# Optimization experiments

Hardware: AMD Instinct MI355X
Metric: run time of the kernel (lower is better)

Reference implementation:

```python
import jax, jax.numpy as jnp
import numpy as np
from jax import lax

B, NCH, T = 256, 32, 2000
NTF, NSF, NSUB, TK = 4, 40, 20, 25
NCLS = 4
NTAN = NSUB * (NSUB + 1) // 2
REIG_EPS = 1e-4


def setup_inputs() -> dict:
    key = jax.random.key(0)
    ks = jax.random.split(key, 8)
    x = jax.random.normal(ks[0], (B, NCH, T), dtype=jnp.float32)
    conv1_w = jax.random.normal(ks[1], (NTF, 1, 1, TK), dtype=jnp.float32) * 0.2
    conv1_b = jnp.zeros((NTF,), dtype=jnp.float32)
    conv2_w = jax.random.normal(ks[2], (NSF, NTF, NCH, 1), dtype=jnp.float32) * 0.1
    conv2_b = jnp.zeros((NSF,), dtype=jnp.float32)
    # BiMap weight: semi-orthogonal (n_subspace x n_spatial_filters) via QR
    A = jax.random.normal(ks[3], (NSF, NSUB), dtype=jnp.float32)
    Q, _ = jnp.linalg.qr(A)
    W_bimap = Q.T  # (NSUB, NSF), rows orthonormal
    clf_w = jax.random.normal(ks[4], (NCLS, NTAN), dtype=jnp.float32) * 0.05
    clf_b = jnp.zeros((NCLS,), dtype=jnp.float32)
    return {"x": x, "conv1_w": conv1_w, "conv1_b": conv1_b,
            "conv2_w": conv2_w, "conv2_b": conv2_b,
            "W_bimap": W_bimap, "clf_w": clf_w, "clf_b": clf_b}


def _forward(x, conv1_w, conv1_b, conv2_w, conv2_b, W_bimap, clf_w, clf_b):
    dn = ('NCHW', 'OIHW', 'NCHW')
    h = x[:, None, :, :]  # (B,1,NCH,T)
    # temporal conv, 'same' with reflect padding along time
    pl = (TK - 1) // 2
    pr = TK - 1 - pl
    hp = jnp.pad(h, ((0, 0), (0, 0), (0, 0), (pl, pr)), mode='reflect')
    h1 = lax.conv_general_dilated(hp, conv1_w, (1, 1), 'VALID', dimension_numbers=dn)
    h1 = h1 + conv1_b[None, :, None, None]  # (B,NTF,NCH,T)
    # spatial conv collapses channel axis
    h2 = lax.conv_general_dilated(h1, conv2_w, (1, 1), 'VALID', dimension_numbers=dn)
    h2 = h2 + conv2_b[None, :, None, None]  # (B,NSF,1,T)
    h2 = h2.reshape(B, NSF, T)
    # covariance pooling over time (unbiased)
    hm = h2 - h2.mean(axis=-1, keepdims=True)
    C = jnp.einsum('bft,bgt->bfg', hm, hm) / (T - 1)  # (B,NSF,NSF)
    # BiMap: S = W C W^T  -> (B,NSUB,NSUB)
    S = jnp.einsum('if,bfg,jg->bij', W_bimap, C, W_bimap)
    # ReEig: clamp eigenvalues at threshold
    w, U = jnp.linalg.eigh(S)
    w = jnp.maximum(w, REIG_EPS)
    S = jnp.einsum('bik,bk,bjk->bij', U, w, U)
    # LogEig: matrix log, take scaled upper triangle, flatten
    w2, U2 = jnp.linalg.eigh(S)
    L = jnp.einsum('bik,bk,bjk->bij', U2, jnp.log(w2), U2)
    iu, ju = jnp.triu_indices(NSUB)
    scale = jnp.where(iu == ju, 1.0, jnp.sqrt(2.0)).astype(L.dtype)
    z = L[:, iu, ju] * scale[None, :]  # (B, NTAN)
    return z @ clf_w.T + clf_b


def reference(x, conv1_w, conv1_b, conv2_w, conv2_b, W_bimap, clf_w, clf_b):
    return _forward(x, conv1_w, conv1_b, conv2_w, conv2_b, W_bimap, clf_w, clf_b)
```

## Files before the change

### kernel.cpp

```cpp
#include <hip/hip_runtime.h>
#include <math.h>

#define B_    256
#define NCH   32
#define T_    2000
#define NTF   4
#define NSF   40
#define NSUB  20
#define TK    25
#define NCLS  4
#define NTAN  210
#define NPAIR 820
#define ACC_STRIDE 860
#define TILE_T 250
#define NTILE  8
#define PL     12

#define ACC_FLOATS (B_*ACC_STRIDE)
#define W2T_OFF ACC_FLOATS
#define W1T_OFF (ACC_FLOATS + NSF*NTF*NCH)

#define XS_TSTR 36
#define H2_STR  252
#define LDS_DW  10080

typedef float v2f __attribute__((ext_vector_type(2)));

__device__ __forceinline__ v2f fma2(v2f a, v2f b, v2f c) {
#if __has_builtin(__builtin_elementwise_fma)
    return __builtin_elementwise_fma(a, b, c);
#else
    v2f r; r.x = fmaf(a.x, b.x, c.x); r.y = fmaf(a.y, b.y, c.y); return r;
#endif
}

__device__ __forceinline__ int pack_ut(int f, int g) {
    return f*NSF - (f*(f-1))/2 + (g - f);
}

__global__ void prep_kernel(const float* __restrict__ conv1_w,
                            const float* __restrict__ conv2_w,
                            float* __restrict__ ws) {
    int tid = threadIdx.x;
    float* w2t = ws + W2T_OFF;
    float* w1t = ws + W1T_OFF;
    for (int i = tid; i < NSF*NTF*NCH; i += 256) {
        int f  = i & 3;
        int sc = i >> 2;
        int c  = sc & 31;
        int s  = sc >> 5;
        w2t[i] = conv2_w[(s*NTF + f)*NCH + c];
    }
    for (int i = tid; i < NTF*TK; i += 256) {
        int f = i & 3;
        int k = i >> 2;
        w1t[i] = conv1_w[f*TK + k];
    }
}

__global__ __launch_bounds__(256, 2)
void conv_gram_kernel(const float* __restrict__ x,
                      const float* __restrict__ conv1_b,
                      const float* __restrict__ conv2_b,
                      const float* __restrict__ wts,
                      float* __restrict__ acc)
{
    __shared__ float lds[LDS_DW];

    const int tid  = threadIdx.x;
    const int bid  = blockIdx.x;
    const int b    = bid >> 3;
    const int tile = bid & 7;
    const int t0   = tile * TILE_T;

    const float* xb = x + (size_t)b*NCH*T_;
    for (int li = tid; li < NCH*280; li += 256) {
        int c = li / 280;
        int i = li - c*280;
        int tg = t0 + i - PL;
        tg = (tg < 0) ? -tg : tg;
        tg = (tg >= T_) ? (2*T_ - 2 - tg) : tg;
        lds[i*XS_TSTR + c] = xb[c*T_ + tg];
    }
    __syncthreads();

    const float4* w1t = (const float4*)(wts + W1T_OFF);
    const float4* w2t = (const float4*)(wts + W2T_OFF);

    v2f h1[64];
    {
        float b0 = conv1_b[0], b1 = conv1_b[1], b2 = conv1_b[2], b3 = conv1_b[3];
        #pragma unroll
        for (int c = 0; c < NCH; ++c) {
            v2f lo; lo.x = b0; lo.y = b1;
            v2f hi; hi.x = b2; hi.y = b3;
            h1[2*c]   = lo;
            h1[2*c+1] = hi;
        }
    }
    #pragma clang loop unroll(disable)
    for (int k = 0; k < TK; ++k) {
        float4 wq = w1t[k];
        v2f w01; w01.x = wq.x; w01.y = wq.y;
        v2f w23; w23.x = wq.z; w23.y = wq.w;
        const float4* xr = (const float4*)&lds[(tid + k)*XS_TSTR];
        float4 xv4[8];
        #pragma unroll
        for (int j = 0; j < 8; ++j) xv4[j] = xr[j];
        const float* xv = (const float*)xv4;
        #pragma unroll
        for (int c = 0; c < NCH; ++c) {
            v2f xc; xc.x = xv[c]; xc.y = xv[c];
            h1[2*c]   = fma2(xc, w01, h1[2*c]);
            h1[2*c+1] = fma2(xc, w23, h1[2*c+1]);
        }
    }
    __syncthreads();

    #pragma clang loop unroll_count(2)
    for (int s = 0; s < NSF; ++s) {
        v2f a01; a01.x = conv2_b[s]; a01.y = 0.f;
        v2f a23; a23.x = 0.f;        a23.y = 0.f;
        #pragma unroll
        for (int c = 0; c < NCH; ++c) {
            float4 wq = w2t[s*NCH + c];
            v2f w01; w01.x = wq.x; w01.y = wq.y;
            v2f w23; w23.x = wq.z; w23.y = wq.w;
            a01 = fma2(w01, h1[2*c],   a01);
            a23 = fma2(w23, h1[2*c+1], a23);
        }
        float v = (a01.x + a01.y) + (a23.x + a23.y);
        if (tid < H2_STR) lds[s*H2_STR + tid] = (tid < TILE_T) ? v : 0.f;
    }
    __syncthreads();

    float* accb = acc + b*ACC_STRIDE;

    if (tid < 55) {
        int bf = 0, rem = tid;
        while (rem >= 10 - bf) { rem -= 10 - bf; bf++; }
        int bg = bf + rem;

        const float4* rA[4];
        const float4* rB[4];
        #pragma unroll
        for (int a = 0; a < 4; ++a) {
            rA[a] = (const float4*)&lds[(4*bf + a)*H2_STR];
            rB[a] = (const float4*)&lds[(4*bg + a)*H2_STR];
        }
        v2f accL[16], accH[16];
        #pragma unroll
        for (int i = 0; i < 16; ++i) { accL[i] = (v2f)0.f; accH[i] = (v2f)0.f; }

        #pragma unroll 7
        for (int q = 0; q < H2_STR/4; ++q) {
            float4 av[4], bv[4];
            #pragma unroll
            for (int a = 0; a < 4; ++a) av[a] = rA[a][q];
            #pragma unroll
            for (int a = 0; a < 4; ++a) bv[a] = rB[a][q];
            #pragma unroll
            for (int a = 0; a < 4; ++a) {
                v2f aL; aL.x = av[a].x; aL.y = av[a].y;
                v2f aH; aH.x = av[a].z; aH.y = av[a].w;
                #pragma unroll
                for (int g = 0; g < 4; ++g) {
                    v2f bL; bL.x = bv[g].x; bL.y = bv[g].y;
                    v2f bH; bH.x = bv[g].z; bH.y = bv[g].w;
                    accL[a*4+g] = fma2(aL, bL, accL[a*4+g]);
                    accH[a*4+g] = fma2(aH, bH, accH[a*4+g]);
                }
            }
        }
        #pragma unroll
        for (int a = 0; a < 4; ++a) {
            #pragma unroll
            for (int g = 0; g < 4; ++g) {
                int f  = 4*bf + a;
                int gg = 4*bg + g;
                if (f <= gg) {
                    v2f sL = accL[a*4+g], sH = accH[a*4+g];
                    float s = (sL.x + sL.y) + (sH.x + sH.y);
                    atomicAdd(&accb[pack_ut(f, gg)], s);
                }
            }
        }
    }

    if (tid >= 64 && tid < 64 + NSF) {
        int row = tid - 64;
        const float4* rr = (const float4*)&lds[row*H2_STR];
        float csum = 0.f;
        #pragma unroll 7
        for (int q = 0; q < H2_STR/4; ++q) {
            float4 v = rr[q];
            csum += (v.x + v.y) + (v.z + v.w);
        }
        atomicAdd(&accb[NPAIR + row], csum);
    }
}

__device__ __forceinline__ void pq_sched(int r, int k, int& p, int& q) {
    if (k == 0) { p = 19; q = r; }
    else {
        int a = r + k;      if (a >= 19) a -= 19;
        int d = r - k + 19; if (d >= 19) d -= 19;
        p = a; q = d;
    }
}

__global__ __launch_bounds__(128)
void finalize_kernel(const float* __restrict__ acc,
                     const float* __restrict__ W_bimap,
                     const float* __restrict__ clf_w,
                     const float* __restrict__ clf_b,
                     float* __restrict__ out)
{
    __shared__ float C[NSF*NSF];
    __shared__ float Wb[NSUB*NSF];
    __shared__ float M[NSUB*NSF];
    __shared__ float A[NSUB*21];
    __shared__ float V[NSUB*21];
    __shared__ float cs_c[10], cs_s[10];
    __shared__ float lam[NSUB];
    __shared__ float z[NTAN];

    const int tid = threadIdx.x;
    const int b   = blockIdx.x;
    const float* accb = acc + b*ACC_STRIDE;

    for (int i = tid; i < NSF*NSF; i += 128) {
        int f = i / NSF, g = i % NSF;
        int lo = f < g ? f : g;
        int hi = f < g ? g : f;
        double G  = (double)accb[pack_ut(lo, hi)];
        double sf = (double)accb[NPAIR + f];
        double sg = (double)accb[NPAIR + g];
        C[i] = (float)((G - sf*sg/(double)T_) / (double)(T_ - 1));
    }
    for (int i = tid; i < NSUB*NSF; i += 128) Wb[i] = W_bimap[i];
    __syncthreads();

    for (int i = tid; i < NSUB*NSF; i += 128) {
        int r = i / NSF, g = i % NSF;
        float s = 0.f;
        #pragma unroll 8
        for (int f = 0; f < NSF; ++f) s = fmaf(Wb[r*NSF+f], C[f*NSF+g], s);
        M[i] = s;
    }
    __syncthreads();

    for (int i = tid; i < NSUB*NSUB; i += 128) {
        int r = i / NSUB, j = i % NSUB;
        float s = 0.f;
        #pragma unroll 8
        for (int g = 0; g < NSF; ++g) s = fmaf(M[r*NSF+g], Wb[j*NSF+g], s);
        A[r*21+j] = s;
        V[r*21+j] = (r == j) ? 1.f : 0.f;
    }
    __syncthreads();

    const int kk = tid / 10;
    const int ll = tid - 10*(tid/10);

    for (int sweep = 0; sweep < 7; ++sweep) {
        for (int r = 0; r < 19; ++r) {
            if (tid < 10) {
                int p, q; pq_sched(r, tid, p, q);
                float app = A[p*21+p], aqq = A[q*21+q], apq = A[p*21+q];
                float c = 1.f, s = 0.f;
                if (fabsf(apq) > 1e-30f) {
                    float tau = (aqq - app) / (2.f*apq);
                    float t = 1.f / (fabsf(tau) + sqrtf(1.f + tau*tau));
                    if (tau < 0.f) t = -t;
                    c = 1.f / sqrtf(1.f + t*t);
                    s = t * c;
                }
                cs_c[tid] = c; cs_s[tid] = s;
            }
            __syncthreads();
            if (tid < 100) {
                int pk, qk, pl, ql;
                pq_sched(r, kk, pk, qk);
                pq_sched(r, ll, pl, ql);
                float ck = cs_c[kk], sk = cs_s[kk];
                float cl = cs_c[ll], sl = cs_s[ll];
                float a00 = A[pk*21+pl], a01 = A[pk*21+ql];
                float a10 = A[qk*21+pl], a11 = A[qk*21+ql];
                float t00 = ck*a00 - sk*a10, t01 = ck*a01 - sk*a11;
                float t10 = sk*a00 + ck*a10, t11 = sk*a01 + ck*a11;
                A[pk*21+pl] = cl*t00 - sl*t01;
                A[pk*21+ql] = sl*t00 + cl*t01;
                A[qk*21+pl] = cl*t10 - sl*t11;
                A[qk*21+ql] = sl*t10 + cl*t11;
                float v00 = V[pk*21+pl], v01 = V[pk*21+ql];
                float v10 = V[qk*21+pl], v11 = V[qk*21+ql];
                V[pk*21+pl] = cl*v00 - sl*v01;
                V[pk*21+ql] = sl*v00 + cl*v01;
                V[qk*21+pl] = cl*v10 - sl*v11;
                V[qk*21+ql] = sl*v10 + cl*v11;
            }
            __syncthreads();
        }
    }

    if (tid < NSUB) {
        float w = A[tid*21+tid];
        lam[tid] = logf(fmaxf(w, 1e-4f));
    }
    __syncthreads();

    for (int p = tid; p < NTAN; p += 128) {
        int i = 0, rem = p;
        while (rem >= NSUB - i) { rem -= NSUB - i; i++; }
        int j = i + rem;
        float s = 0.f;
        #pragma unroll 5
        for (int k = 0; k < NSUB; ++k) s = fmaf(V[i*21+k]*lam[k], V[j*21+k], s);
        z[p] = (i == j) ? s : s * 1.41421356237309515f;
    }
    __syncthreads();

    if (tid < NCLS) {
        float s = clf_b[tid];
        for (int p = 0; p < NTAN; ++p) s = fmaf(clf_w[tid*NTAN+p], z[p], s);
        out[b*NCLS + tid] = s;
    }
}

extern "C" void kernel_launch(void* const* d_in, const int* in_sizes, int n_in,
                              void* d_out, int out_size, void* d_ws, size_t ws_size,
                              hipStream_t stream) {
    const float* x       = (const float*)d_in[0];
    const float* conv1_w = (const float*)d_in[1];
    const float* conv1_b = (const float*)d_in[2];
    const float* conv2_w = (const float*)d_in[3];
    const float* conv2_b = (const float*)d_in[4];
    const float* W_bimap = (const float*)d_in[5];
    const float* clf_w   = (const float*)d_in[6];
    const float* clf_b   = (const float*)d_in[7];
    float* out = (float*)d_out;
    float* ws  = (float*)d_ws;

    hipMemsetAsync(ws, 0, (size_t)ACC_FLOATS*sizeof(float), stream);

    prep_kernel<<<1, 256, 0, stream>>>(conv1_w, conv2_w, ws);
    conv_gram_kernel<<<B_*NTILE, 256, 0, stream>>>(x, conv1_b, conv2_b, ws, ws);
    finalize_kernel<<<B_, 128, 0, stream>>>(ws, W_bimap, clf_w, clf_b, out);
}
```

Baseline: 329.4 us.

## Restructure conv into channel groups, split gram across 220 threads, single-wave Jacobi finalize

The conv stage now processes channels in groups of 8, folding each group's temporal conv straight into 40 running spatial-conv accumulators. This drops the 64-register h1 array, which should lower register pressure. The Gram stage now spreads the 55 tile pairs across four time chunks each (220 threads) instead of 55 threads, and the column sums likewise use 160 threads, at the cost of more atomics. The finalize kernel runs as a single 64-thread wave that computes rotation coefficients redundantly per thread with fast rcp/rsq intrinsics, which removes one barrier per Jacobi round. That last part may cost some precision.

Result: slower. 714.3 us (+116.8%).

```diff
diff --git a/kernel.cpp b/kernel.cpp
--- a/kernel.cpp
+++ b/kernel.cpp
@@ -21,8 +21,8 @@
 #define W1T_OFF (ACC_FLOATS + NSF*NTF*NCH)
 
 #define XS_TSTR 36
-#define H2_STR  252
-#define LDS_DW  10080
+#define H2_STR  260
+#define LDS_DW  10400
 
 typedef float v2f __attribute__((ext_vector_type(2)));
 
@@ -87,73 +87,90 @@
     const float4* w1t = (const float4*)(wts + W1T_OFF);
     const float4* w2t = (const float4*)(wts + W2T_OFF);
 
-    v2f h1[64];
-    {
-        float b0 = conv1_b[0], b1 = conv1_b[1], b2 = conv1_b[2], b3 = conv1_b[3];
+    float h2acc[NSF];
+    #pragma unroll
+    for (int s = 0; s < NSF; ++s) h2acc[s] = conv2_b[s];
+
+    const float b1_0 = conv1_b[0], b1_1 = conv1_b[1], b1_2 = conv1_b[2], b1_3 = conv1_b[3];
+
+    for (int g = 0; g < 4; ++g) {
+        v2f h1g[16];
         #pragma unroll
-        for (int c = 0; c < NCH; ++c) {
-            v2f lo; lo.x = b0; lo.y = b1;
-            v2f hi; hi.x = b2; hi.y = b3;
-            h1[2*c]   = lo;
-            h1[2*c+1] = hi;
-        }
-    }
-    #pragma clang loop unroll(disable)
-    for (int k = 0; k < TK; ++k) {
-        float4 wq = w1t[k];
-        v2f w01; w01.x = wq.x; w01.y = wq.y;
-        v2f w23; w23.x = wq.z; w23.y = wq.w;
-        const float4* xr = (const float4*)&lds[(tid + k)*XS_TSTR];
-        float4 xv4[8];
-        #pragma unroll
-        for (int j = 0; j < 8; ++j) xv4[j] = xr[j];
-        const float* xv = (const float*)xv4;
-        #pragma unroll
-        for (int c = 0; c < NCH; ++c) {
-            v2f xc; xc.x = xv[c]; xc.y = xv[c];
-            h1[2*c]   = fma2(xc, w01, h1[2*c]);
-            h1[2*c+1] = fma2(xc, w23, h1[2*c+1]);
-        }
-    }
-    __syncthreads();
-
-    #pragma clang loop unroll_count(2)
-    for (int s = 0; s < NSF; ++s) {
-        v2f a01; a01.x = conv2_b[s]; a01.y = 0.f;
-        v2f a23; a23.x = 0.f;        a23.y = 0.f;
-        #pragma unroll
-        for (int c = 0; c < NCH; ++c) {
-            float4 wq = w2t[s*NCH + c];
+        for (int c = 0; c < 8; ++c) {
+            v2f lo; lo.x = b1_0; lo.y = b1_1;
+            v2f hi; hi.x = b1_2; hi.y = b1_3;
+            h1g[2*c]   = lo;
+            h1g[2*c+1] = hi;
+        }
+        #pragma clang loop unroll(disable)
+        for (int k = 0; k < TK; ++k) {
+            float4 wq = w1t[k];
             v2f w01; w01.x = wq.x; w01.y = wq.y;
             v2f w23; w23.x = wq.z; w23.y = wq.w;
-            a01 = fma2(w01, h1[2*c],   a01);
-            a23 = fma2(w23, h1[2*c+1], a23);
-        }
-        float v = (a01.x + a01.y) + (a23.x + a23.y);
-        if (tid < H2_STR) lds[s*H2_STR + tid] = (tid < TILE_T) ? v : 0.f;
+            const float4* xp = (const float4*)&lds[(tid + k)*XS_TSTR + 8*g];
+            float4 xa = xp[0];
+            float4 xc = xp[1];
+            float xv0 = xa.x, xv1 = xa.y, xv2 = xa.z, xv3 = xa.w;
+            float xv4 = xc.x, xv5 = xc.y, xv6 = xc.z, xv7 = xc.w;
+            v2f t;
+            t.x = xv0; t.y = xv0; h1g[0]  = fma2(t, w01, h1g[0]);  h1g[1]  = fma2(t, w23, h1g[1]);
+            t.x = xv1; t.y = xv1; h1g[2]  = fma2(t, w01, h1g[2]);  h1g[3]  = fma2(t, w23, h1g[3]);
+            t.x = xv2; t.y = xv2; h1g[4]  = fma2(t, w01, h1g[4]);  h1g[5]  = fma2(t, w23, h1g[5]);
+            t.x = xv3; t.y = xv3; h1g[6]  = fma2(t, w01, h1g[6]);  h1g[7]  = fma2(t, w23, h1g[7]);
+            t.x = xv4; t.y = xv4; h1g[8]  = fma2(t, w01, h1g[8]);  h1g[9]  = fma2(t, w23, h1g[9]);
+            t.x = xv5; t.y = xv5; h1g[10] = fma2(t, w01, h1g[10]); h1g[11] = fma2(t, w23, h1g[11]);
+            t.x = xv6; t.y = xv6; h1g[12] = fma2(t, w01, h1g[12]); h1g[13] = fma2(t, w23, h1g[13]);
+            t.x = xv7; t.y = xv7; h1g[14] = fma2(t, w01, h1g[14]); h1g[15] = fma2(t, w23, h1g[15]);
+        }
+        #pragma unroll
+        for (int s = 0; s < NSF; ++s) {
+            v2f a2; a2.x = 0.f; a2.y = 0.f;
+            #pragma unroll
+            for (int c = 0; c < 8; ++c) {
+                float4 wq = w2t[s*NCH + 8*g + c];
+                v2f w01; w01.x = wq.x; w01.y = wq.y;
+                v2f w23; w23.x = wq.z; w23.y = wq.w;
+                a2 = fma2(w01, h1g[2*c],   a2);
+                a2 = fma2(w23, h1g[2*c+1], a2);
+            }
+            h2acc[s] += a2.x + a2.y;
+        }
+    }
+    __syncthreads();
+
+    #pragma unroll
+    for (int s = 0; s < NSF; ++s) {
+        float vw = (tid < TILE_T) ? h2acc[s] : 0.f;
+        lds[s*H2_STR + tid] = vw;
+    }
+    for (int i = tid; i < NSF*4; i += 256) {
+        int s = i >> 2, col = 256 + (i & 3);
+        lds[s*H2_STR + col] = 0.f;
     }
     __syncthreads();
 
     float* accb = acc + b*ACC_STRIDE;
 
-    if (tid < 55) {
-        int bf = 0, rem = tid;
+    if (tid < 220) {
+        int tilei = tid >> 2, chunk = tid & 3;
+        int bf = 0, rem = tilei;
         while (rem >= 10 - bf) { rem -= 10 - bf; bf++; }
         int bg = bf + rem;
+        int q0 = chunk * 16;
+        int qn = (chunk == 3) ? 17 : 16;
 
         const float4* rA[4];
         const float4* rB[4];
         #pragma unroll
         for (int a = 0; a < 4; ++a) {
-            rA[a] = (const float4*)&lds[(4*bf + a)*H2_STR];
-            rB[a] = (const float4*)&lds[(4*bg + a)*H2_STR];
+            rA[a] = (const float4*)&lds[(bf + 10*a)*H2_STR] + q0;
+            rB[a] = (const float4*)&lds[(bg + 10*a)*H2_STR] + q0;
         }
         v2f accL[16], accH[16];
         #pragma unroll
-        for (int i = 0; i < 16; ++i) { accL[i] = (v2f)0.f; accH[i] = (v2f)0.f; }
-
-        #pragma unroll 7
-        for (int q = 0; q < H2_STR/4; ++q) {
+        for (int i = 0; i < 16; ++i) { accL[i].x = 0.f; accL[i].y = 0.f; accH[i] = accL[i]; }
+
+        for (int q = 0; q < qn; ++q) {
             float4 av[4], bv[4];
             #pragma unroll
             for (int a = 0; a < 4; ++a) av[a] = rA[a][q];
@@ -164,39 +181,42 @@
                 v2f aL; aL.x = av[a].x; aL.y = av[a].y;
                 v2f aH; aH.x = av[a].z; aH.y = av[a].w;
                 #pragma unroll
-                for (int g = 0; g < 4; ++g) {
-                    v2f bL; bL.x = bv[g].x; bL.y = bv[g].y;
-                    v2f bH; bH.x = bv[g].z; bH.y = bv[g].w;
-                    accL[a*4+g] = fma2(aL, bL, accL[a*4+g]);
-                    accH[a*4+g] = fma2(aH, bH, accH[a*4+g]);
+                for (int gI = 0; gI < 4; ++gI) {
+                    v2f bL; bL.x = bv[gI].x; bL.y = bv[gI].y;
+                    v2f bH; bH.x = bv[gI].z; bH.y = bv[gI].w;
+                    accL[a*4+gI] = fma2(aL, bL, accL[a*4+gI]);
+                    accH[a*4+gI] = fma2(aH, bH, accH[a*4+gI]);
                 }
             }
         }
         #pragma unroll
         for (int a = 0; a < 4; ++a) {
             #pragma unroll
-            for (int g = 0; g < 4; ++g) {
-                int f  = 4*bf + a;
-                int gg = 4*bg + g;
-                if (f <= gg) {
-                    v2f sL = accL[a*4+g], sH = accH[a*4+g];
+            for (int gI = 0; gI < 4; ++gI) {
+                int f  = bf + 10*a;
+                int gg = bg + 10*gI;
+                if (bf != bg || a <= gI) {
+                    int lo = f < gg ? f : gg;
+                    int hi = f < gg ? gg : f;
+                    v2f sL = accL[a*4+gI], sH = accH[a*4+gI];
                     float s = (sL.x + sL.y) + (sH.x + sH.y);
-                    atomicAdd(&accb[pack_ut(f, gg)], s);
+                    atomicAdd(&accb[pack_ut(lo, hi)], s);
                 }
             }
         }
     }
 
-    if (tid >= 64 && tid < 64 + NSF) {
-        int row = tid - 64;
-        const float4* rr = (const float4*)&lds[row*H2_STR];
-        float csum = 0.f;
-        #pragma unroll 7
-        for (int q = 0; q < H2_STR/4; ++q) {
+    if (tid < 160) {
+        int row = tid >> 2, chunk = tid & 3;
+        int q0 = chunk * 16;
+        int qn = (chunk == 3) ? 17 : 16;
+        const float4* rr = (const float4*)&lds[row*H2_STR] + q0;
+        float cs = 0.f;
+        for (int q = 0; q < qn; ++q) {
             float4 v = rr[q];
-            csum += (v.x + v.y) + (v.z + v.w);
-        }
-        atomicAdd(&accb[NPAIR + row], csum);
+            cs += (v.x + v.y) + (v.z + v.w);
+        }
+        atomicAdd(&accb[NPAIR + row], cs);
     }
 }
 
@@ -209,7 +229,19 @@
     }
 }
 
-__global__ __launch_bounds__(128)
+__device__ __forceinline__ void rotcs(float app, float aqq, float apq,
+                                      float& c, float& s) {
+    if (fabsf(apq) > 1e-30f) {
+        float tau = (aqq - app) * __builtin_amdgcn_rcpf(2.f*apq);
+        float sq  = __builtin_amdgcn_sqrtf(fmaf(tau, tau, 1.f));
+        float t   = __builtin_amdgcn_rcpf(fabsf(tau) + sq);
+        t = (tau < 0.f) ? -t : t;
+        c = __builtin_amdgcn_rsqf(fmaf(t, t, 1.f));
+        s = t * c;
+    } else { c = 1.f; s = 0.f; }
+}
+
+__global__ __launch_bounds__(64)
 void finalize_kernel(const float* __restrict__ acc,
                      const float* __restrict__ W_bimap,
                      const float* __restrict__ clf_w,
@@ -221,7 +253,6 @@
     __shared__ float M[NSUB*NSF];
     __shared__ float A[NSUB*21];
     __shared__ float V[NSUB*21];
-    __shared__ float cs_c[10], cs_s[10];
     __shared__ float lam[NSUB];
     __shared__ float z[NTAN];
 
@@ -229,19 +260,19 @@
     const int b   = blockIdx.x;
     const float* accb = acc + b*ACC_STRIDE;
 
-    for (int i = tid; i < NSF*NSF; i += 128) {
+    for (int i = tid; i < NSF*NSF; i += 64) {
         int f = i / NSF, g = i % NSF;
         int lo = f < g ? f : g;
         int hi = f < g ? g : f;
         double G  = (double)accb[pack_ut(lo, hi)];
         double sf = (double)accb[NPAIR + f];
         double sg = (double)accb[NPAIR + g];
-        C[i] = (float)((G - sf*sg/(double)T_) / (double)(T_ - 1));
-    }
-    for (int i = tid; i < NSUB*NSF; i += 128) Wb[i] = W_bimap[i];
-    __syncthreads();
-
-    for (int i = tid; i < NSUB*NSF; i += 128) {
+        C[i] = (float)((G - sf*sg*(1.0/2000.0)) * (1.0/1999.0));
+    }
+    for (int i = tid; i < NSUB*NSF; i += 64) Wb[i] = W_bimap[i];
+    __syncthreads();
+
+    for (int i = tid; i < NSUB*NSF; i += 64) {
         int r = i / NSF, g = i % NSF;
         float s = 0.f;
         #pragma unroll 8
@@ -250,7 +281,7 @@
     }
     __syncthreads();
 
-    for (int i = tid; i < NSUB*NSUB; i += 128) {
+    for (int i = tid; i < NSUB*NSUB; i += 64) {
         int r = i / NSUB, j = i % NSUB;
         float s = 0.f;
         #pragma unroll 8
@@ -260,45 +291,67 @@
     }
     __syncthreads();
 
-    const int kk = tid / 10;
-    const int ll = tid - 10*(tid/10);
+    const int k0 = tid / 10, l0 = tid - 10*(tid/10);
+    const bool has1 = (tid < 36);
+    const int i1 = tid + 64;
+    const int k1 = i1 / 10, l1 = i1 - 10*(i1/10);
 
     for (int sweep = 0; sweep < 7; ++sweep) {
         for (int r = 0; r < 19; ++r) {
-            if (tid < 10) {
-                int p, q; pq_sched(r, tid, p, q);
-                float app = A[p*21+p], aqq = A[q*21+q], apq = A[p*21+q];
-                float c = 1.f, s = 0.f;
-                if (fabsf(apq) > 1e-30f) {
-                    float tau = (aqq - app) / (2.f*apq);
-                    float t = 1.f / (fabsf(tau) + sqrtf(1.f + tau*tau));
-                    if (tau < 0.f) t = -t;
-                    c = 1.f / sqrtf(1.f + t*t);
-                    s = t * c;
-                }
-                cs_c[tid] = c; cs_s[tid] = s;
-            }
-            __syncthreads();
-            if (tid < 100) {
-                int pk, qk, pl, ql;
-                pq_sched(r, kk, pk, qk);
-                pq_sched(r, ll, pl, ql);
-                float ck = cs_c[kk], sk = cs_s[kk];
-                float cl = cs_c[ll], sl = cs_s[ll];
-                float a00 = A[pk*21+pl], a01 = A[pk*21+ql];
-                float a10 = A[qk*21+pl], a11 = A[qk*21+ql];
-                float t00 = ck*a00 - sk*a10, t01 = ck*a01 - sk*a11;
-                float t10 = sk*a00 + ck*a10, t11 = sk*a01 + ck*a11;
-                A[pk*21+pl] = cl*t00 - sl*t01;
-                A[pk*21+ql] = sl*t00 + cl*t01;
-                A[qk*21+pl] = cl*t10 - sl*t11;
-                A[qk*21+ql] = sl*t10 + cl*t11;
-                float v00 = V[pk*21+pl], v01 = V[pk*21+ql];
-                float v10 = V[qk*21+pl], v11 = V[qk*21+ql];
-                V[pk*21+pl] = cl*v00 - sl*v01;
-                V[pk*21+ql] = sl*v00 + cl*v01;
-                V[qk*21+pl] = cl*v10 - sl*v11;
-                V[qk*21+ql] = sl*v10 + cl*v11;
+            int pk0, qk0, pl0, ql0, pk1, qk1, pl1, ql1;
+            pq_sched(r, k0, pk0, qk0);
+            pq_sched(r, l0, pl0, ql0);
+            pq_sched(r, k1, pk1, qk1);
+            pq_sched(r, l1, pl1, ql1);
+
+            float kpp0 = A[pk0*21+pk0], kqq0 = A[qk0*21+qk0], kpq0 = A[pk0*21+qk0];
+            float lpp0 = A[pl0*21+pl0], lqq0 = A[ql0*21+ql0], lpq0 = A[pl0*21+ql0];
+            float a00_0 = A[pk0*21+pl0], a01_0 = A[pk0*21+ql0];
+            float a10_0 = A[qk0*21+pl0], a11_0 = A[qk0*21+ql0];
+            float v00_0 = V[pk0*21+pl0], v01_0 = V[pk0*21+ql0];
+            float v10_0 = V[qk0*21+pl0], v11_0 = V[qk0*21+ql0];
+
+            float kpp1=0.f, kqq1=0.f, kpq1=0.f, lpp1=0.f, lqq1=0.f, lpq1=0.f;
+            float a00_1=0.f, a01_1=0.f, a10_1=0.f, a11_1=0.f;
+            float v00_1=0.f, v01_1=0.f, v10_1=0.f, v11_1=0.f;
+            if (has1) {
+                kpp1 = A[pk1*21+pk1]; kqq1 = A[qk1*21+qk1]; kpq1 = A[pk1*21+qk1];
+                lpp1 = A[pl1*21+pl1]; lqq1 = A[ql1*21+ql1]; lpq1 = A[pl1*21+ql1];
+                a00_1 = A[pk1*21+pl1]; a01_1 = A[pk1*21+ql1];
+                a10_1 = A[qk1*21+pl1]; a11_1 = A[qk1*21+ql1];
+                v00_1 = V[pk1*21+pl1]; v01_1 = V[pk1*21+ql1];
+                v10_1 = V[qk1*21+pl1]; v11_1 = V[qk1*21+ql1];
+            }
+
+            float ck0, sk0, cl0, sl0, ck1, sk1, cl1, sl1;
+            rotcs(kpp0, kqq0, kpq0, ck0, sk0);
+            rotcs(lpp0, lqq0, lpq0, cl0, sl0);
+            rotcs(kpp1, kqq1, kpq1, ck1, sk1);
+            rotcs(lpp1, lqq1, lpq1, cl1, sl1);
+
+            {
+                float t00 = ck0*a00_0 - sk0*a10_0, t01 = ck0*a01_0 - sk0*a11_0;
+                float t10 = sk0*a00_0 + ck0*a10_0, t11 = sk0*a01_0 + ck0*a11_0;
+                A[pk0*21+pl0] = cl0*t00 - sl0*t01;
+                A[pk0*21+ql0] = sl0*t00 + cl0*t01;
+                A[qk0*21+pl0] = cl0*t10 - sl0*t11;
+                A[qk0*21+ql0] = sl0*t10 + cl0*t11;
+                V[pk0*21+pl0] = cl0*v00_0 - sl0*v01_0;
+                V[pk0*21+ql0] = sl0*v00_0 + cl0*v01_0;
+                V[qk0*21+pl0] = cl0*v10_0 - sl0*v11_0;
+                V[qk0*21+ql0] = sl0*v10_0 + cl0*v11_0;
+            }
+            if (has1) {
+                float t00 = ck1*a00_1 - sk1*a10_1, t01 = ck1*a01_1 - sk1*a11_1;
+                float t10 = sk1*a00_1 + ck1*a10_1, t11 = sk1*a01_1 + ck1*a11_1;
+                A[pk1*21+pl1] = cl1*t00 - sl1*t01;
+                A[pk1*21+ql1] = sl1*t00 + cl1*t01;
+                A[qk1*21+pl1] = cl1*t10 - sl1*t11;
+                A[qk1*21+ql1] = sl1*t10 + cl1*t11;
+                V[pk1*21+pl1] = cl1*v00_1 - sl1*v01_1;
+                V[pk1*21+ql1] = sl1*v00_1 + cl1*v01_1;
+                V[qk1*21+pl1] = cl1*v10_1 - sl1*v11_1;
+                V[qk1*21+ql1] = sl1*v10_1 + cl1*v11_1;
             }
             __syncthreads();
         }
@@ -310,7 +363,7 @@
     }
     __syncthreads();
 
-    for (int p = tid; p < NTAN; p += 128) {
+    for (int p = tid; p < NTAN; p += 64) {
         int i = 0, rem = p;
         while (rem >= NSUB - i) { rem -= NSUB - i; i++; }
         int j = i + rem;
@@ -346,5 +399,5 @@
 
     prep_kernel<<<1, 256, 0, stream>>>(conv1_w, conv2_w, ws);
     conv_gram_kernel<<<B_*NTILE, 256, 0, stream>>>(x, conv1_b, conv2_b, ws, ws);
-    finalize_kernel<<<B_, 128, 0, stream>>>(ws, W_bimap, clf_w, clf_b, out);
-}
+    finalize_kernel<<<B_, 64, 0, stream>>>(ws, W_bimap, clf_w, clf_b, out);
+}
```

## Replace atomics with per-tile partials, widen Gram split, single-wave Jacobi with shuffles

Applied to the files above, without the earlier changes.

The conv/Gram kernel now writes per-tile partial sums to workspace instead of atomically accumulating, which removes the memset. The Gram product is spread over 210 threads with 2x2 output blocks instead of 55 threads with 4x4, and a 4-tile, two-pass fallback is selected when the workspace is too small. The finalize kernel runs as a single 64-thread wave: it reduces the partials, uses precomputed index tables and lane shuffles for the rotation coefficients, and replaces divisions with fast reciprocal intrinsics. It also cuts the number of Jacobi sweeps from 7 to 6, which risks lower eigenvalue accuracy.

Measured after the change: 423.0 us. 28.4% more time.

```diff
diff --git a/kernel.cpp b/kernel.cpp
--- a/kernel.cpp
+++ b/kernel.cpp
@@ -11,18 +11,16 @@
 #define NCLS  4
 #define NTAN  210
 #define NPAIR 820
-#define ACC_STRIDE 860
-#define TILE_T 250
-#define NTILE  8
-#define PL     12
-
-#define ACC_FLOATS (B_*ACC_STRIDE)
-#define W2T_OFF ACC_FLOATS
-#define W1T_OFF (ACC_FLOATS + NSF*NTF*NCH)
+#define PL    12
+
+#define W2T_OFF 0
+#define W1T_OFF 5120
+#define PART_OFF 5248
+#define PART_STRIDE 864
 
 #define XS_TSTR 36
-#define H2_STR  252
-#define LDS_DW  10080
+#define H2_STR  260
+#define LDS_DW  10400
 
 typedef float v2f __attribute__((ext_vector_type(2)));
 
@@ -63,141 +61,142 @@
                       const float* __restrict__ conv1_b,
                       const float* __restrict__ conv2_b,
                       const float* __restrict__ wts,
-                      float* __restrict__ acc)
+                      float* __restrict__ part)
 {
     __shared__ float lds[LDS_DW];
 
-    const int tid  = threadIdx.x;
-    const int bid  = blockIdx.x;
-    const int b    = bid >> 3;
-    const int tile = bid & 7;
-    const int t0   = tile * TILE_T;
+    const int tid   = threadIdx.x;
+    const int bid   = blockIdx.x;
+    const int ntile = gridDim.x >> 8;
+    const int sh    = (ntile == 8) ? 3 : 2;
+    const int b     = bid >> sh;
+    const int tile  = bid & (ntile - 1);
+    const int npass = (ntile == 8) ? 1 : 2;
 
     const float* xb = x + (size_t)b*NCH*T_;
-    for (int li = tid; li < NCH*280; li += 256) {
-        int c = li / 280;
-        int i = li - c*280;
-        int tg = t0 + i - PL;
-        tg = (tg < 0) ? -tg : tg;
-        tg = (tg >= T_) ? (2*T_ - 2 - tg) : tg;
-        lds[i*XS_TSTR + c] = xb[c*T_ + tg];
-    }
-    __syncthreads();
-
     const float4* w1t = (const float4*)(wts + W1T_OFF);
     const float4* w2t = (const float4*)(wts + W2T_OFF);
 
-    v2f h1[64];
-    {
-        float b0 = conv1_b[0], b1 = conv1_b[1], b2 = conv1_b[2], b3 = conv1_b[3];
-        #pragma unroll
-        for (int c = 0; c < NCH; ++c) {
-            v2f lo; lo.x = b0; lo.y = b1;
-            v2f hi; hi.x = b2; hi.y = b3;
-            h1[2*c]   = lo;
-            h1[2*c+1] = hi;
-        }
-    }
+    int bf = 0, bg = 0;
+    if (tid < 210) {
+        int rem = tid;
+        while (rem >= NSUB - bf) { rem -= NSUB - bf; bf++; }
+        bg = bf + rem;
+    }
+    float4 e00 = make_float4(0,0,0,0), e01 = e00, e10 = e00, e11 = e00;
+    float csum = 0.f;
+    const int scol = tid - 216;
+    const bool isCol = (tid >= 216);
+
     #pragma clang loop unroll(disable)
-    for (int k = 0; k < TK; ++k) {
-        float4 wq = w1t[k];
-        v2f w01; w01.x = wq.x; w01.y = wq.y;
-        v2f w23; w23.x = wq.z; w23.y = wq.w;
-        const float4* xr = (const float4*)&lds[(tid + k)*XS_TSTR];
-        float4 xv4[8];
-        #pragma unroll
-        for (int j = 0; j < 8; ++j) xv4[j] = xr[j];
-        const float* xv = (const float*)xv4;
-        #pragma unroll
-        for (int c = 0; c < NCH; ++c) {
-            v2f xc; xc.x = xv[c]; xc.y = xv[c];
-            h1[2*c]   = fma2(xc, w01, h1[2*c]);
-            h1[2*c+1] = fma2(xc, w23, h1[2*c+1]);
-        }
-    }
-    __syncthreads();
-
-    #pragma clang loop unroll_count(2)
-    for (int s = 0; s < NSF; ++s) {
-        v2f a01; a01.x = conv2_b[s]; a01.y = 0.f;
-        v2f a23; a23.x = 0.f;        a23.y = 0.f;
-        #pragma unroll
-        for (int c = 0; c < NCH; ++c) {
-            float4 wq = w2t[s*NCH + c];
+    for (int pass = 0; pass < npass; ++pass) {
+        const int t0 = (tile*npass + pass) * 250;
+        __syncthreads();
+
+        for (int li = tid; li < NCH*280; li += 256) {
+            int c = li / 280;
+            int i = li - c*280;
+            int tg = t0 + i - PL;
+            tg = (tg < 0) ? -tg : tg;
+            tg = (tg >= T_) ? (2*T_ - 2 - tg) : tg;
+            lds[i*XS_TSTR + c] = xb[c*T_ + tg];
+        }
+        __syncthreads();
+
+        v2f h1[64];
+        {
+            float b0 = conv1_b[0], b1 = conv1_b[1], b2 = conv1_b[2], b3 = conv1_b[3];
+            #pragma unroll
+            for (int c = 0; c < NCH; ++c) {
+                v2f lo; lo.x = b0; lo.y = b1;
+                v2f hi; hi.x = b2; hi.y = b3;
+                h1[2*c]   = lo;
+                h1[2*c+1] = hi;
+            }
+        }
+        #pragma clang loop unroll(disable)
+        for (int k = 0; k < TK; ++k) {
+            float4 wq = w1t[k];
             v2f w01; w01.x = wq.x; w01.y = wq.y;
             v2f w23; w23.x = wq.z; w23.y = wq.w;
-            a01 = fma2(w01, h1[2*c],   a01);
-            a23 = fma2(w23, h1[2*c+1], a23);
-        }
-        float v = (a01.x + a01.y) + (a23.x + a23.y);
-        if (tid < H2_STR) lds[s*H2_STR + tid] = (tid < TILE_T) ? v : 0.f;
-    }
-    __syncthreads();
-
-    float* accb = acc + b*ACC_STRIDE;
-
-    if (tid < 55) {
-        int bf = 0, rem = tid;
-        while (rem >= 10 - bf) { rem -= 10 - bf; bf++; }
-        int bg = bf + rem;
-
-        const float4* rA[4];
-        const float4* rB[4];
-        #pragma unroll
-        for (int a = 0; a < 4; ++a) {
-            rA[a] = (const float4*)&lds[(4*bf + a)*H2_STR];
-            rB[a] = (const float4*)&lds[(4*bg + a)*H2_STR];
-        }
-        v2f accL[16], accH[16];
-        #pragma unroll
-        for (int i = 0; i < 16; ++i) { accL[i] = (v2f)0.f; accH[i] = (v2f)0.f; }
-
-        #pragma unroll 7
-        for (int q = 0; q < H2_STR/4; ++q) {
-            float4 av[4], bv[4];
+            const float4* xr = (const float4*)&lds[(tid + k)*XS_TSTR];
+            float4 xv4[8];
             #pragma unroll
-            for (int a = 0; a < 4; ++a) av[a] = rA[a][q];
+            for (int j = 0; j < 8; ++j) xv4[j] = xr[j];
             #pragma unroll
-            for (int a = 0; a < 4; ++a) bv[a] = rB[a][q];
+            for (int j = 0; j < 8; ++j) {
+                float4 xq = xv4[j];
+                v2f t;
+                t.x = xq.x; t.y = xq.x; h1[8*j+0] = fma2(t, w01, h1[8*j+0]); h1[8*j+1] = fma2(t, w23, h1[8*j+1]);
+                t.x = xq.y; t.y = xq.y; h1[8*j+2] = fma2(t, w01, h1[8*j+2]); h1[8*j+3] = fma2(t, w23, h1[8*j+3]);
+                t.x = xq.z; t.y = xq.z; h1[8*j+4] = fma2(t, w01, h1[8*j+4]); h1[8*j+5] = fma2(t, w23, h1[8*j+5]);
+                t.x = xq.w; t.y = xq.w; h1[8*j+6] = fma2(t, w01, h1[8*j+6]); h1[8*j+7] = fma2(t, w23, h1[8*j+7]);
+            }
+        }
+        __syncthreads();
+
+        #pragma clang loop unroll_count(2)
+        for (int s = 0; s < NSF; ++s) {
+            v2f a01; a01.x = conv2_b[s]; a01.y = 0.f;
+            v2f a23; a23.x = 0.f;        a23.y = 0.f;
             #pragma unroll
-            for (int a = 0; a < 4; ++a) {
-                v2f aL; aL.x = av[a].x; aL.y = av[a].y;
-                v2f aH; aH.x = av[a].z; aH.y = av[a].w;
-                #pragma unroll
-                for (int g = 0; g < 4; ++g) {
-                    v2f bL; bL.x = bv[g].x; bL.y = bv[g].y;
-                    v2f bH; bH.x = bv[g].z; bH.y = bv[g].w;
-                    accL[a*4+g] = fma2(aL, bL, accL[a*4+g]);
-                    accH[a*4+g] = fma2(aH, bH, accH[a*4+g]);
-                }
-            }
-        }
-        #pragma unroll
-        for (int a = 0; a < 4; ++a) {
-            #pragma unroll
-            for (int g = 0; g < 4; ++g) {
-                int f  = 4*bf + a;
-                int gg = 4*bg + g;
-                if (f <= gg) {
-                    v2f sL = accL[a*4+g], sH = accH[a*4+g];
-                    float s = (sL.x + sL.y) + (sH.x + sH.y);
-                    atomicAdd(&accb[pack_ut(f, gg)], s);
-                }
-            }
-        }
-    }
-
-    if (tid >= 64 && tid < 64 + NSF) {
-        int row = tid - 64;
-        const float4* rr = (const float4*)&lds[row*H2_STR];
-        float csum = 0.f;
-        #pragma unroll 7
-        for (int q = 0; q < H2_STR/4; ++q) {
-            float4 v = rr[q];
-            csum += (v.x + v.y) + (v.z + v.w);
-        }
-        atomicAdd(&accb[NPAIR + row], csum);
-    }
+            for (int c = 0; c < NCH; ++c) {
+                float4 wq = w2t[s*NCH + c];
+                v2f w01; w01.x = wq.x; w01.y = wq.y;
+                v2f w23; w23.x = wq.z; w23.y = wq.w;
+                a01 = fma2(w01, h1[2*c],   a01);
+                a23 = fma2(w23, h1[2*c+1], a23);
+            }
+            float v = (a01.x + a01.y) + (a23.x + a23.y);
+            lds[s*H2_STR + tid] = (tid < 250) ? v : 0.f;
+        }
+        for (int i = tid; i < NSF*4; i += 256) {
+            int s = i >> 2;
+            lds[s*H2_STR + 256 + (i & 3)] = 0.f;
+        }
+        __syncthreads();
+
+        if (tid < 210) {
+            const float4* r0 = (const float4*)&lds[(2*bf  )*H2_STR];
+            const float4* r1 = (const float4*)&lds[(2*bf+1)*H2_STR];
+            const float4* r2 = (const float4*)&lds[(2*bg  )*H2_STR];
+            const float4* r3 = (const float4*)&lds[(2*bg+1)*H2_STR];
+            #pragma unroll 5
+            for (int q = 0; q < H2_STR/4; ++q) {
+                float4 a0 = r0[q], a1 = r1[q], b0 = r2[q], b1 = r3[q];
+                e00.x = fmaf(a0.x, b0.x, e00.x); e00.y = fmaf(a0.y, b0.y, e00.y);
+                e00.z = fmaf(a0.z, b0.z, e00.z); e00.w = fmaf(a0.w, b0.w, e00.w);
+                e01.x = fmaf(a0.x, b1.x, e01.x); e01.y = fmaf(a0.y, b1.y, e01.y);
+                e01.z = fmaf(a0.z, b1.z, e01.z); e01.w = fmaf(a0.w, b1.w, e01.w);
+                e10.x = fmaf(a1.x, b0.x, e10.x); e10.y = fmaf(a1.y, b0.y, e10.y);
+                e10.z = fmaf(a1.z, b0.z, e10.z); e10.w = fmaf(a1.w, b0.w, e10.w);
+                e11.x = fmaf(a1.x, b1.x, e11.x); e11.y = fmaf(a1.y, b1.y, e11.y);
+                e11.z = fmaf(a1.z, b1.z, e11.z); e11.w = fmaf(a1.w, b1.w, e11.w);
+            }
+        }
+        if (isCol) {
+            const float4* rr = (const float4*)&lds[scol*H2_STR];
+            #pragma unroll 5
+            for (int q = 0; q < H2_STR/4; ++q) {
+                float4 v = rr[q];
+                csum += (v.x + v.y) + (v.z + v.w);
+            }
+        }
+    }
+
+    float* pb = part + (size_t)bid * PART_STRIDE;
+    if (tid < 210) {
+        int f0 = 2*bf, f1 = 2*bf+1, g0 = 2*bg, g1 = 2*bg+1;
+        float s00 = (e00.x+e00.y)+(e00.z+e00.w);
+        float s01 = (e01.x+e01.y)+(e01.z+e01.w);
+        float s10 = (e10.x+e10.y)+(e10.z+e10.w);
+        float s11 = (e11.x+e11.y)+(e11.z+e11.w);
+        pb[pack_ut(f0,g0)] = s00;
+        pb[pack_ut(f0,g1)] = s01;
+        if (bf != bg) pb[pack_ut(f1,g0)] = s10;
+        pb[pack_ut(f1,g1)] = s11;
+    }
+    if (isCol) pb[NPAIR + scol] = csum;
 }
 
 __device__ __forceinline__ void pq_sched(int r, int k, int& p, int& q) {
@@ -209,39 +208,86 @@
     }
 }
 
-__global__ __launch_bounds__(128)
-void finalize_kernel(const float* __restrict__ acc,
+__device__ __forceinline__ void rotcs(float app, float aqq, float apq,
+                                      float& c, float& s) {
+    if (fabsf(apq) > 1e-30f) {
+        float tau = (aqq - app) * __builtin_amdgcn_rcpf(2.f*apq);
+        float sq  = __builtin_amdgcn_sqrtf(fmaf(tau, tau, 1.f));
+        float t   = __builtin_amdgcn_rcpf(fabsf(tau) + sq);
+        t = (tau < 0.f) ? -t : t;
+        c = __builtin_amdgcn_rsqf(fmaf(t, t, 1.f));
+        s = t * c;
+    } else { c = 1.f; s = 0.f; }
+}
+
+__global__ __launch_bounds__(64)
+void finalize_kernel(const float* __restrict__ part,
                      const float* __restrict__ W_bimap,
                      const float* __restrict__ clf_w,
                      const float* __restrict__ clf_b,
-                     float* __restrict__ out)
+                     float* __restrict__ out,
+                     int ntile)
 {
+    __shared__ float Gacc[PART_STRIDE];
     __shared__ float C[NSF*NSF];
     __shared__ float Wb[NSUB*NSF];
     __shared__ float M[NSUB*NSF];
     __shared__ float A[NSUB*21];
     __shared__ float V[NSUB*21];
-    __shared__ float cs_c[10], cs_s[10];
     __shared__ float lam[NSUB];
     __shared__ float z[NTAN];
+    __shared__ int4 tab0[19*64];
+    __shared__ int4 tab1[19*36];
+    __shared__ int4 tabR[19*10];
 
     const int tid = threadIdx.x;
     const int b   = blockIdx.x;
-    const float* accb = acc + b*ACC_STRIDE;
-
-    for (int i = tid; i < NSF*NSF; i += 128) {
+
+    for (int i = tid; i < NPAIR + NSF; i += 64) {
+        double s = 0.0;
+        for (int t = 0; t < ntile; ++t)
+            s += (double)part[(size_t)(b*ntile + t)*PART_STRIDE + i];
+        Gacc[i] = (float)s;
+    }
+    for (int i = tid; i < NSUB*NSF; i += 64) Wb[i] = W_bimap[i];
+
+    for (int i = tid; i < 19*64; i += 64) {
+        int r = i >> 6, it = i & 63;
+        int k = it / 10, l = it - 10*k;
+        int pk, qk, pl, ql;
+        pq_sched(r, k, pk, qk);
+        pq_sched(r, l, pl, ql);
+        tab0[i] = make_int4(pk*21+pl, pk*21+ql, qk*21+pl, qk*21+ql);
+    }
+    for (int i = tid; i < 19*36; i += 64) {
+        int r = i / 36, t = i - 36*r;
+        int it = t + 64;
+        int k = it / 10, l = it - 10*k;
+        int pk, qk, pl, ql;
+        pq_sched(r, k, pk, qk);
+        pq_sched(r, l, pl, ql);
+        tab1[i] = make_int4(pk*21+pl, pk*21+ql, qk*21+pl, qk*21+ql);
+    }
+    for (int i = tid; i < 19*10; i += 64) {
+        int r = i / 10, k = i - 10*r;
+        int p, q;
+        pq_sched(r, k, p, q);
+        tabR[i] = make_int4(p*21+p, q*21+q, p*21+q, 0);
+    }
+    __syncthreads();
+
+    for (int i = tid; i < NSF*NSF; i += 64) {
         int f = i / NSF, g = i % NSF;
         int lo = f < g ? f : g;
         int hi = f < g ? g : f;
-        double G  = (double)accb[pack_ut(lo, hi)];
-        double sf = (double)accb[NPAIR + f];
-        double sg = (double)accb[NPAIR + g];
-        C[i] = (float)((G - sf*sg/(double)T_) / (double)(T_ - 1));
-    }
-    for (int i = tid; i < NSUB*NSF; i += 128) Wb[i] = W_bimap[i];
-    __syncthreads();
-
-    for (int i = tid; i < NSUB*NSF; i += 128) {
+        double G  = (double)Gacc[pack_ut(lo, hi)];
+        double sf = (double)Gacc[NPAIR + f];
+        double sg = (double)Gacc[NPAIR + g];
+        C[i] = (float)((G - sf*sg*(1.0/2000.0)) * (1.0/1999.0));
+    }
+    __syncthreads();
+
+    for (int i = tid; i < NSUB*NSF; i += 64) {
         int r = i / NSF, g = i % NSF;
         float s = 0.f;
         #pragma unroll 8
@@ -250,7 +296,7 @@
     }
     __syncthreads();
 
-    for (int i = tid; i < NSUB*NSUB; i += 128) {
+    for (int i = tid; i < NSUB*NSUB; i += 64) {
         int r = i / NSUB, j = i % NSUB;
         float s = 0.f;
         #pragma unroll 8
@@ -260,45 +306,58 @@
     }
     __syncthreads();
 
-    const int kk = tid / 10;
-    const int ll = tid - 10*(tid/10);
-
-    for (int sweep = 0; sweep < 7; ++sweep) {
+    const int m0 = tid - 10*(tid/10);
+    const int k0 = tid / 10;
+    const bool has1 = (tid < 36);
+    const int it1 = tid + 64;
+    const int k1 = it1 / 10, l1 = it1 - 10*(it1/10);
+
+    for (int sweep = 0; sweep < 6; ++sweep) {
         for (int r = 0; r < 19; ++r) {
-            if (tid < 10) {
-                int p, q; pq_sched(r, tid, p, q);
-                float app = A[p*21+p], aqq = A[q*21+q], apq = A[p*21+q];
-                float c = 1.f, s = 0.f;
-                if (fabsf(apq) > 1e-30f) {
-                    float tau = (aqq - app) / (2.f*apq);
-                    float t = 1.f / (fabsf(tau) + sqrtf(1.f + tau*tau));
-                    if (tau < 0.f) t = -t;
-                    c = 1.f / sqrtf(1.f + t*t);
-                    s = t * c;
-                }
-                cs_c[tid] = c; cs_s[tid] = s;
-            }
-            __syncthreads();
-            if (tid < 100) {
-                int pk, qk, pl, ql;
-                pq_sched(r, kk, pk, qk);
-                pq_sched(r, ll, pl, ql);
-                float ck = cs_c[kk], sk = cs_s[kk];
-                float cl = cs_c[ll], sl = cs_s[ll];
-                float a00 = A[pk*21+pl], a01 = A[pk*21+ql];
-                float a10 = A[qk*21+pl], a11 = A[qk*21+ql];
-                float t00 = ck*a00 - sk*a10, t01 = ck*a01 - sk*a11;
-                float t10 = sk*a00 + ck*a10, t11 = sk*a01 + ck*a11;
-                A[pk*21+pl] = cl*t00 - sl*t01;
-                A[pk*21+ql] = sl*t00 + cl*t01;
-                A[qk*21+pl] = cl*t10 - sl*t11;
-                A[qk*21+ql] = sl*t10 + cl*t11;
-                float v00 = V[pk*21+pl], v01 = V[pk*21+ql];
-                float v10 = V[qk*21+pl], v11 = V[qk*21+ql];
-                V[pk*21+pl] = cl*v00 - sl*v01;
-                V[pk*21+ql] = sl*v00 + cl*v01;
-                V[qk*21+pl] = cl*v10 - sl*v11;
-                V[qk*21+ql] = sl*v10 + cl*v11;
+            int4 ro = tabR[r*10 + m0];
+            float app = A[ro.x], aqq = A[ro.y], apq = A[ro.z];
+            float c, s;
+            rotcs(app, aqq, apq, c, s);
+            float cl0 = c, sl0 = s;
+            float ck0 = __shfl(c, k0), sk0 = __shfl(s, k0);
+            float ck1 = __shfl(c, k1), sk1 = __shfl(s, k1);
+            float cl1 = __shfl(c, l1), sl1 = __shfl(s, l1);
+
+            int4 o0 = tab0[r*64 + tid];
+            float a00 = A[o0.x], a01 = A[o0.y], a10 = A[o0.z], a11 = A[o0.w];
+            float v00 = V[o0.x], v01 = V[o0.y], v10 = V[o0.z], v11 = V[o0.w];
+
+            int4 o1 = tab1[r*36 + (has1 ? tid : 0)];
+            float b00=0.f, b01=0.f, b10=0.f, b11=0.f;
+            float w00=0.f, w01v=0.f, w10=0.f, w11=0.f;
+            if (has1) {
+                b00 = A[o1.x]; b01 = A[o1.y]; b10 = A[o1.z]; b11 = A[o1.w];
+                w00 = V[o1.x]; w01v = V[o1.y]; w10 = V[o1.z]; w11 = V[o1.w];
+            }
+
+            {
+                float t00 = ck0*a00 - sk0*a10, t01 = ck0*a01 - sk0*a11;
+                float t10 = sk0*a00 + ck0*a10, t11 = sk0*a01 + ck0*a11;
+                A[o0.x] = cl0*t00 - sl0*t01;
+                A[o0.y] = sl0*t00 + cl0*t01;
+                A[o0.z] = cl0*t10 - sl0*t11;
+                A[o0.w] = sl0*t10 + cl0*t11;
+                V[o0.x] = cl0*v00 - sl0*v01;
+                V[o0.y] = sl0*v00 + cl0*v01;
+                V[o0.z] = cl0*v10 - sl0*v11;
+                V[o0.w] = sl0*v10 + cl0*v11;
+            }
+            if (has1) {
+                float t00 = ck1*b00 - sk1*b10, t01 = ck1*b01 - sk1*b11;
+                float t10 = sk1*b00 + ck1*b10, t11 = sk1*b01 + ck1*b11;
+                A[o1.x] = cl1*t00 - sl1*t01;
+                A[o1.y] = sl1*t00 + cl1*t01;
+                A[o1.z] = cl1*t10 - sl1*t11;
+                A[o1.w] = sl1*t10 + cl1*t11;
+                V[o1.x] = cl1*w00 - sl1*w01v;
+                V[o1.y] = sl1*w00 + cl1*w01v;
+                V[o1.z] = cl1*w10 - sl1*w11;
+                V[o1.w] = sl1*w10 + cl1*w11;
             }
             __syncthreads();
         }
@@ -310,7 +369,7 @@
     }
     __syncthreads();
 
-    for (int p = tid; p < NTAN; p += 128) {
+    for (int p = tid; p < NTAN; p += 64) {
         int i = 0, rem = p;
         while (rem >= NSUB - i) { rem -= NSUB - i; i++; }
         int j = i + rem;
@@ -342,9 +401,10 @@
     float* out = (float*)d_out;
     float* ws  = (float*)d_ws;
 
-    hipMemsetAsync(ws, 0, (size_t)ACC_FLOATS*sizeof(float), stream);
+    const size_t need8 = (size_t)(PART_OFF + 2048*PART_STRIDE) * sizeof(float);
+    const int ntile = (ws_size >= need8) ? 8 : 4;
 
     prep_kernel<<<1, 256, 0, stream>>>(conv1_w, conv2_w, ws);
-    conv_gram_kernel<<<B_*NTILE, 256, 0, stream>>>(x, conv1_b, conv2_b, ws, ws);
-    finalize_kernel<<<B_, 128, 0, stream>>>(ws, W_bimap, clf_w, clf_b, out);
-}
+    conv_gram_kernel<<<B_*ntile, 256, 0, stream>>>(x, conv1_b, conv2_b, ws, ws + PART_OFF);
+    finalize_kernel<<<B_, 64, 0, stream>>>(ws + PART_OFF, W_bimap, clf_w, clf_b, out, ntile);
+}
```
